# Performance work log

Hardware: AMD Instinct MI355X
Metric: run time of the kernel (lower is better)

Reference implementation:

```python
import jax, jax.numpy as jnp
import numpy as np
from jax.scipy.special import logsumexp

EPS = 1e-3
MAX_ITER = 100
THRESH = 0.1

def setup_inputs() -> dict:
    key = jax.random.key(0)
    k1, k2 = jax.random.split(key)
    B, N, M, D = 16, 1024, 1024, 32
    output = jax.random.normal(k1, (B, N, D), dtype=jnp.float32)
    labels = jax.random.normal(k2, (B, M, D), dtype=jnp.float32)
    return {"output": output, "labels": labels}

def _sinkhorn_cost(output, labels):
    # C_ij = sum_d |x_i - y_j|^2, shape [B, N, M]
    C = jnp.sum(jnp.abs(output[..., :, None, :] - labels[..., None, :, :]) ** 2, axis=-1)
    B, N, M = C.shape
    log_mu = jnp.full((B, N), jnp.log(1.0 / N + 1e-8), dtype=C.dtype)
    log_nu = jnp.full((B, M), jnp.log(1.0 / M + 1e-8), dtype=C.dtype)

    def Mmat(u, v):
        # (-C + u_i + v_j) / eps
        return (-C + u[..., :, None] + v[..., None, :]) / EPS

    def step(carry, _):
        u, v, done = carry
        u_new = EPS * (log_mu - logsumexp(Mmat(u, v), axis=-1)) + u
        v_new = EPS * (log_nu - logsumexp(Mmat(u_new, v), axis=-2)) + v
        err = jnp.mean(jnp.sum(jnp.abs(u_new - u), axis=-1))
        # the update that triggers convergence IS applied (torch breaks after update)
        u2 = jnp.where(done, u, u_new)
        v2 = jnp.where(done, v, v_new)
        done = done | (err < THRESH)
        return (u2, v2, done), None

    u0 = jnp.zeros((B, N), dtype=C.dtype)
    v0 = jnp.zeros((B, M), dtype=C.dtype)
    (u, v, _), _ = jax.lax.scan(jax.checkpoint(step), (u0, v0, jnp.asarray(False)), None, length=MAX_ITER)
    pi = jnp.exp(Mmat(u, v))
    cost = jnp.sum(pi * C, axis=(-2, -1))  # [B]
    return jnp.mean(cost)  # reduction='mean'

def reference(output, labels):
    return _sinkhorn_cost(output, labels)
```

## Files before the change

kernel.cpp:

```cpp
#include <hip/hip_runtime.h>

constexpr int   NN       = 1024;
constexpr float EPSf     = 1e-3f;
constexpr int   MAX_ITER = 100;

#define K2      1442.6950408889634f
#define TWOK2   2885.3900817779268f
#define LN2f    0.6931471805599453f
#define INV_LN2 1.4426950408889634f
#define INV_EPS 1000.0f
#define LOGK    (-6.9314616f)

#define EXP2F(x) __builtin_amdgcn_exp2f(x)
#define LOG2F(x) __builtin_amdgcn_logf(x)

typedef _Float16 f16x8 __attribute__((ext_vector_type(8)));
typedef float    f32x4 __attribute__((ext_vector_type(4)));

__device__ __forceinline__ void msmerge(float& ma, float& sa, float mb, float sb)
{
    const float m2 = fmaxf(ma, mb);
    sa = fmaf(sa, EXP2F(ma - m2), sb * EXP2F(mb - m2));
    ma = m2;
}

__global__ __launch_bounds__(256) void prep(
    const float* __restrict__ X, const float* __restrict__ Y,
    _Float16* __restrict__ Xh, _Float16* __restrict__ Yh,
    float* __restrict__ xsq, float* __restrict__ ysq)
{
    const int gid = blockIdx.x * 256 + threadIdx.x;
    const float* src; _Float16* dst; float* sq; int row;
    if (gid < 16384) { src = X; dst = Xh; sq = xsq; row = gid; }
    else             { src = Y; dst = Yh; sq = ysq; row = gid - 16384; }

    const float4* s4 = (const float4*)(src + (size_t)row * 32);
    float acc = 0.f;
#pragma unroll
    for (int i = 0; i < 4; ++i) {
        float4 a = s4[2 * i], b = s4[2 * i + 1];
        acc += a.x*a.x + a.y*a.y + a.z*a.z + a.w*a.w;
        acc += b.x*b.x + b.y*b.y + b.z*b.z + b.w*b.w;
        f16x8 h = {(_Float16)a.x, (_Float16)a.y, (_Float16)a.z, (_Float16)a.w,
                   (_Float16)b.x, (_Float16)b.y, (_Float16)b.z, (_Float16)b.w};
        *(f16x8*)(dst + (size_t)row * 32 + i * 8) = h;
    }
    sq[row] = acc;
}

#define YSLOT(c, k) (((c) << 5) + (((k) ^ (((c) >> 1) & 3)) << 3))

__global__ __launch_bounds__(1024, 1) void lse_mfma_pass(
    const _Float16* __restrict__ Ah,
    const _Float16* __restrict__ Bh,
    const float* __restrict__ asq,
    const float* __restrict__ bsq,
    const float* __restrict__ vin,
    float* __restrict__ vout,
    float* __restrict__ err,
    int* __restrict__ dflag, int it, int do_err)
{
    __shared__ _Float16 Yl[32768];
    __shared__ float    wk[1024];
    __shared__ float    mrg[64][8];
    __shared__ int      s_fb;

    const int tid = threadIdx.x;
    const int b   = blockIdx.x & 15, blk = blockIdx.x >> 4;

    if (!do_err && blockIdx.x == 0 && tid < 16) {
        float e = err[(tid << 7) + it];
        e += __shfl_xor(e, 1); e += __shfl_xor(e, 2);
        e += __shfl_xor(e, 4); e += __shfl_xor(e, 8);
        if (tid == 0) dflag[it + 1] = dflag[it] | (e < 1.6f ? 1 : 0);
    }
    if (dflag[it]) return;
    if (tid == 0) s_fb = 0;

    {
        const float4* src = (const float4*)(Bh + ((size_t)b << 15));
#pragma unroll
        for (int i = 0; i < 4; ++i) {
            const int g = tid + (i << 10);
            const int row = g >> 2, k = g & 3;
            *(float4*)(Yl + YSLOT(row, k)) = src[g];
        }
        const int c = (b << 10) + tid;
        wk[tid] = (vin[c] - bsq[c]) * K2;
    }
    __syncthreads();

    const int wave = tid >> 6, lane = tid & 63;
    const int wr = wave >> 2, wc = wave & 3;
    const int l15 = lane & 15, l4 = lane >> 4;
    const int rowb = (blk << 6) + (wr << 4);

    const f16x8 afrag = *(const f16x8*)(Ah + ((size_t)b << 15) +
                                        ((size_t)(rowb + l15) << 5) + (l4 << 3));
    const float4 xs4 = *(const float4*)(asq + (b << 10) + rowb + (l4 << 2));
    const float4 uo4 = *(const float4*)(vout + (b << 10) + rowb + (l4 << 2));
    const float xk[4] = {xs4.x * K2, xs4.y * K2, xs4.z * K2, xs4.w * K2};
    float xm[4];
    {
        const float u4[4] = {uo4.x, uo4.y, uo4.z, uo4.w};
#pragma unroll
        for (int r = 0; r < 4; ++r)
            xm[r] = xk[r] + (LOGK - u4[r] * INV_EPS) * INV_LN2;
    }

    float wreg[16];
#pragma unroll
    for (int t = 0; t < 16; ++t) wreg[t] = wk[(wc << 8) + (t << 4) + l15];

    float s[4] = {0.f, 0.f, 0.f, 0.f};
#pragma unroll 4
    for (int t = 0; t < 16; ++t) {
        const int col = (wc << 8) + (t << 4) + l15;
        const f16x8 bfrag = *(const f16x8*)(Yl + YSLOT(col, l4));
        f32x4 z = {0.f, 0.f, 0.f, 0.f};
        f32x4 d = __builtin_amdgcn_mfma_f32_16x16x32_f16(afrag, bfrag, z, 0, 0, 0);
#pragma unroll
        for (int r = 0; r < 4; ++r)
            s[r] += EXP2F(fmaf(d[r], TWOK2, wreg[t] - xm[r]));
    }
#pragma unroll
    for (int off = 1; off < 16; off <<= 1)
#pragma unroll
        for (int r = 0; r < 4; ++r) s[r] += __shfl_xor(s[r], off);
    if (l15 == 0) {
#pragma unroll
        for (int r = 0; r < 4; ++r) mrg[(wr << 4) + (l4 << 2) + r][wc] = s[r];
    }
    __syncthreads();

    float S = 0.f, uo = 0.f, M0r = 0.f;
    int gr = 0;
    if (tid < 64) {
        S = mrg[tid][0] + mrg[tid][1] + mrg[tid][2] + mrg[tid][3];
        gr = (b << 10) + (blk << 6) + tid;
        uo = vout[gr];
        M0r = (LOGK - uo * INV_EPS) * INV_LN2;
        if (!(S >= 1e-27f && S <= 1e38f)) s_fb = 1;
    }
    __syncthreads();

    if (!s_fb) {
        if (tid < 64) {
            const float lse2 = M0r + LOG2F(S);
            const float nv = EPSf * (LOGK - lse2 * LN2f);
            float werr = do_err ? fabsf(nv - uo) : 0.f;
            vout[gr] = nv;
#pragma unroll
            for (int off = 32; off > 0; off >>= 1) werr += __shfl_xor(werr, off);
            if (do_err && tid == 0) atomicAdd(err + (b << 7) + it, werr);
        }
        return;
    }

    float m[4] = {-3.4e38f, -3.4e38f, -3.4e38f, -3.4e38f};
    float sf[4] = {0.f, 0.f, 0.f, 0.f};
#pragma unroll 4
    for (int t = 0; t < 16; ++t) {
        const int col = (wc << 8) + (t << 4) + l15;
        const f16x8 bfrag = *(const f16x8*)(Yl + YSLOT(col, l4));
        f32x4 z = {0.f, 0.f, 0.f, 0.f};
        f32x4 d = __builtin_amdgcn_mfma_f32_16x16x32_f16(afrag, bfrag, z, 0, 0, 0);
#pragma unroll
        for (int r = 0; r < 4; ++r) {
            const float arg = fmaf(d[r], TWOK2, wreg[t] - xk[r]);
            const float big = fmaxf(m[r], arg);
            const float e   = EXP2F(fminf(m[r], arg) - big);
            sf[r] = (arg > m[r]) ? fmaf(sf[r], e, 1.0f) : (sf[r] + e);
            m[r] = big;
        }
    }
#pragma unroll
    for (int off = 1; off < 16; off <<= 1)
#pragma unroll
        for (int r = 0; r < 4; ++r)
            msmerge(m[r], sf[r], __shfl_xor(m[r], off), __shfl_xor(sf[r], off));
    if (l15 == 0) {
#pragma unroll
        for (int r = 0; r < 4; ++r) {
            const int rb = (wr << 4) + (l4 << 2) + r;
            mrg[rb][wc]     = m[r];
            mrg[rb][4 + wc] = sf[r];
        }
    }
    __syncthreads();

    if (tid < 64) {
        float M = mrg[tid][0], Sf = mrg[tid][4];
        msmerge(M, Sf, mrg[tid][1], mrg[tid][5]);
        msmerge(M, Sf, mrg[tid][2], mrg[tid][6]);
        msmerge(M, Sf, mrg[tid][3], mrg[tid][7]);
        const float lse2 = M + LOG2F(Sf);
        const float nv = EPSf * (LOGK - lse2 * LN2f);
        float werr = do_err ? fabsf(nv - uo) : 0.f;
        vout[gr] = nv;
#pragma unroll
        for (int off = 32; off > 0; off >>= 1) werr += __shfl_xor(werr, off);
        if (do_err && tid == 0) atomicAdd(err + (b << 7) + it, werr);
    }
}

__global__ __launch_bounds__(1024, 1) void cost_mfma(
    const _Float16* __restrict__ Xh, const _Float16* __restrict__ Yh,
    const float* __restrict__ xsq, const float* __restrict__ ysq,
    const float* __restrict__ u, const float* __restrict__ v,
    float* __restrict__ out)
{
    __shared__ _Float16 Yl[32768];
    __shared__ float red[16];
    const int tid = threadIdx.x;
    const int b   = blockIdx.x & 15, blk = blockIdx.x >> 4;

    {   const float4* src = (const float4*)(Yh + ((size_t)b << 15));
#pragma unroll
        for (int i = 0; i < 4; ++i) {
            const int g = tid + (i << 10);
            const int row = g >> 2, k = g & 3;
            *(float4*)(Yl + YSLOT(row, k)) = src[g];
        }
    }
    __syncthreads();

    const int wave = tid >> 6, lane = tid & 63;
    const int wr = wave >> 2, wc = wave & 3;
    const int l15 = lane & 15, l4 = lane >> 4;
    const int rowb = (blk << 6) + (wr << 4);

    const f16x8 afrag = *(const f16x8*)(Xh + ((size_t)b << 15) +
                                        ((size_t)(rowb + l15) << 5) + (l4 << 3));
    const float4 xs4 = *(const float4*)(xsq + (b << 10) + rowb + (l4 << 2));
    const float xs[4] = {xs4.x, xs4.y, xs4.z, xs4.w};
    const float4 uu4 = *(const float4*)(u + (b << 10) + rowb + (l4 << 2));
    const float uk[4] = {uu4.x * K2, uu4.y * K2, uu4.z * K2, uu4.w * K2};

    float vk[16], ys[16];
#pragma unroll
    for (int t = 0; t < 16; ++t) {
        const int c = (b << 10) + (wc << 8) + (t << 4) + l15;
        vk[t] = v[c] * K2;
        ys[t] = ysq[c];
    }

    float csum = 0.f;
#pragma unroll 4
    for (int t = 0; t < 16; ++t) {
        const int col = (wc << 8) + (t << 4) + l15;
        const f16x8 bfrag = *(const f16x8*)(Yl + YSLOT(col, l4));
        f32x4 z = {0.f, 0.f, 0.f, 0.f};
        f32x4 d = __builtin_amdgcn_mfma_f32_16x16x32_f16(afrag, bfrag, z, 0, 0, 0);
#pragma unroll
        for (int r = 0; r < 4; ++r) {
            const float C   = fmaf(-2.f, d[r], xs[r] + ys[t]);
            const float arg = fmaf(C, -K2, uk[r] + vk[t]);
            csum += EXP2F(arg) * C;
        }
    }
#pragma unroll
    for (int off = 32; off > 0; off >>= 1) csum += __shfl_xor(csum, off);

    if (lane == 0) red[wave] = csum;
    __syncthreads();
    if (tid == 0) {
        float tot = 0.f;
#pragma unroll
        for (int w = 0; w < 16; ++w) tot += red[w];
        atomicAdd(out, tot * (1.0f / 16.0f));
    }
}

extern "C" void kernel_launch(void* const* d_in, const int* in_sizes, int n_in,
                              void* d_out, int out_size, void* d_ws, size_t ws_size,
                              hipStream_t stream) {
    const float* x = (const float*)d_in[0];
    const float* y = (const float*)d_in[1];

    char* wsb = (char*)d_ws;
    _Float16* Xh = (_Float16*)wsb;
    _Float16* Yh = (_Float16*)(wsb + (1u << 20));
    float* xsq   = (float*)(wsb + (2u << 20));
    float* ysq   = xsq + 16384;
    float* u     = ysq + 16384;
    float* v     = u + 16384;
    float* err   = v + 16384;
    int*   dflag = (int*)(err + 2048);
    float* out   = (float*)d_out;

    (void)hipMemsetAsync(u, 0, (size_t)(2 * 16384 + 2048 + 128) * 4, stream);
    (void)hipMemsetAsync(out, 0, sizeof(float), stream);

    prep<<<dim3(128), dim3(256), 0, stream>>>(x, y, Xh, Yh, xsq, ysq);

    for (int it = 0; it < MAX_ITER; ++it) {
        lse_mfma_pass<<<dim3(256), dim3(1024), 0, stream>>>(
            Xh, Yh, xsq, ysq, v, u, err, dflag, it, 1);
        lse_mfma_pass<<<dim3(256), dim3(1024), 0, stream>>>(
            Yh, Xh, ysq, xsq, u, v, err, dflag, it, 0);
    }

    cost_mfma<<<dim3(256), dim3(1024), 0, stream>>>(Xh, Yh, xsq, ysq, u, v, out);
}
```

Before: 1.362 ms.

## Fuse u and v Sinkhorn half-steps into one kernel via column partial logsumexp

```diff
diff --git a/kernel.cpp b/kernel.cpp
--- a/kernel.cpp
+++ b/kernel.cpp
@@ -50,43 +50,61 @@
 
 #define YSLOT(c, k) (((c) << 5) + (((k) ^ (((c) >> 1) & 3)) << 3))
 
-__global__ __launch_bounds__(1024, 1) void lse_mfma_pass(
-    const _Float16* __restrict__ Ah,
-    const _Float16* __restrict__ Bh,
-    const float* __restrict__ asq,
-    const float* __restrict__ bsq,
-    const float* __restrict__ vin,
-    float* __restrict__ vout,
+__global__ __launch_bounds__(1024, 1) void sink_iter(
+    const _Float16* __restrict__ Xh, const _Float16* __restrict__ Yh,
+    const float* __restrict__ xsq, const float* __restrict__ ysq,
+    float* __restrict__ u,
+    float2* __restrict__ Sp,
     float* __restrict__ err,
-    int* __restrict__ dflag, int it, int do_err)
+    int it)
 {
     __shared__ _Float16 Yl[32768];
-    __shared__ float    wk[1024];
-    __shared__ float    mrg[64][8];
-    __shared__ int      s_fb;
+    __shared__ float  wk[1024];
+    __shared__ float  bks[1024];
+    __shared__ float  mrg[64][8];
+    __shared__ float2 colp[4][1024];
+    __shared__ float  unew[64];
+    __shared__ int    s_fb, s_frz;
 
     const int tid = threadIdx.x;
     const int b   = blockIdx.x & 15, blk = blockIdx.x >> 4;
 
-    if (!do_err && blockIdx.x == 0 && tid < 16) {
-        float e = err[(tid << 7) + it];
-        e += __shfl_xor(e, 1); e += __shfl_xor(e, 2);
-        e += __shfl_xor(e, 4); e += __shfl_xor(e, 8);
-        if (tid == 0) dflag[it + 1] = dflag[it] | (e < 1.6f ? 1 : 0);
-    }
-    if (dflag[it]) return;
+    if (it > 0) {
+        if (tid == 0) {
+            float e = 0.f;
+            const float* ep = err + (it - 1) * 16;
+#pragma unroll
+            for (int q = 0; q < 16; ++q) e += ep[q];
+            s_frz = (e < 1.6f) ? 1 : 0;
+        }
+        __syncthreads();
+        if (s_frz) return;
+    }
     if (tid == 0) s_fb = 0;
 
     {
-        const float4* src = (const float4*)(Bh + ((size_t)b << 15));
+        const float4* src = (const float4*)(Yh + ((size_t)b << 15));
 #pragma unroll
         for (int i = 0; i < 4; ++i) {
             const int g = tid + (i << 10);
             const int row = g >> 2, k = g & 3;
             *(float4*)(Yl + YSLOT(row, k)) = src[g];
         }
-        const int c = (b << 10) + tid;
-        wk[tid] = (vin[c] - bsq[c]) * K2;
+        float vj = 0.f;
+        if (it > 0) {
+            const float2* sp = Sp + ((size_t)b << 14) + tid;
+            float2 p0 = sp[0];
+            float M = p0.x, S = p0.y;
+#pragma unroll
+            for (int k = 1; k < 16; ++k) {
+                float2 p = sp[k << 10];
+                msmerge(M, S, p.x, p.y);
+            }
+            vj = EPSf * (LOGK - (M + LOG2F(S)) * LN2f);
+        }
+        const float bq = ysq[(b << 10) + tid];
+        wk[tid]  = (vj - bq) * K2;
+        bks[tid] = bq * K2;
     }
     __syncthreads();
 
@@ -95,19 +113,17 @@
     const int l15 = lane & 15, l4 = lane >> 4;
     const int rowb = (blk << 6) + (wr << 4);
 
-    const f16x8 afrag = *(const f16x8*)(Ah + ((size_t)b << 15) +
+    const f16x8 afrag = *(const f16x8*)(Xh + ((size_t)b << 15) +
                                         ((size_t)(rowb + l15) << 5) + (l4 << 3));
-    const float4 xs4 = *(const float4*)(asq + (b << 10) + rowb + (l4 << 2));
-    const float4 uo4 = *(const float4*)(vout + (b << 10) + rowb + (l4 << 2));
+    const float4 xs4 = *(const float4*)(xsq + (b << 10) + rowb + (l4 << 2));
+    const float4 uo4 = *(const float4*)(u + (b << 10) + rowb + (l4 << 2));
     const float xk[4] = {xs4.x * K2, xs4.y * K2, xs4.z * K2, xs4.w * K2};
     float xm[4];
-    {
-        const float u4[4] = {uo4.x, uo4.y, uo4.z, uo4.w};
+    {   const float u4[4] = {uo4.x, uo4.y, uo4.z, uo4.w};
 #pragma unroll
         for (int r = 0; r < 4; ++r)
             xm[r] = xk[r] + (LOGK - u4[r] * INV_EPS) * INV_LN2;
     }
-
     float wreg[16];
 #pragma unroll
     for (int t = 0; t < 16; ++t) wreg[t] = wk[(wc << 8) + (t << 4) + l15];
@@ -138,7 +154,7 @@
     if (tid < 64) {
         S = mrg[tid][0] + mrg[tid][1] + mrg[tid][2] + mrg[tid][3];
         gr = (b << 10) + (blk << 6) + tid;
-        uo = vout[gr];
+        uo = u[gr];
         M0r = (LOGK - uo * INV_EPS) * INV_LN2;
         if (!(S >= 1e-27f && S <= 1e38f)) s_fb = 1;
     }
@@ -146,19 +162,74 @@
 
     if (!s_fb) {
         if (tid < 64) {
-            const float lse2 = M0r + LOG2F(S);
-            const float nv = EPSf * (LOGK - lse2 * LN2f);
-            float werr = do_err ? fabsf(nv - uo) : 0.f;
-            vout[gr] = nv;
+            const float nv = EPSf * (LOGK - (M0r + LOG2F(S)) * LN2f);
+            unew[tid] = nv;
+            u[gr] = nv;
+            float werr = fabsf(nv - uo);
 #pragma unroll
             for (int off = 32; off > 0; off >>= 1) werr += __shfl_xor(werr, off);
-            if (do_err && tid == 0) atomicAdd(err + (b << 7) + it, werr);
-        }
-        return;
-    }
-
-    float m[4] = {-3.4e38f, -3.4e38f, -3.4e38f, -3.4e38f};
-    float sf[4] = {0.f, 0.f, 0.f, 0.f};
+            if (tid == 0) atomicAdd(err + it * 16 + b, werr);
+        }
+    } else {
+        float m[4] = {-3.4e38f, -3.4e38f, -3.4e38f, -3.4e38f};
+        float sf[4] = {0.f, 0.f, 0.f, 0.f};
+#pragma unroll 4
+        for (int t = 0; t < 16; ++t) {
+            const int col = (wc << 8) + (t << 4) + l15;
+            const f16x8 bfrag = *(const f16x8*)(Yl + YSLOT(col, l4));
+            f32x4 z = {0.f, 0.f, 0.f, 0.f};
+            f32x4 d = __builtin_amdgcn_mfma_f32_16x16x32_f16(afrag, bfrag, z, 0, 0, 0);
+#pragma unroll
+            for (int r = 0; r < 4; ++r) {
+                const float arg = fmaf(d[r], TWOK2, wreg[t] - xk[r]);
+                const float big = fmaxf(m[r], arg);
+                const float e   = EXP2F(fminf(m[r], arg) - big);
+                sf[r] = (arg > m[r]) ? fmaf(sf[r], e, 1.0f) : (sf[r] + e);
+                m[r] = big;
+            }
+        }
+#pragma unroll
+        for (int off = 1; off < 16; off <<= 1)
+#pragma unroll
+            for (int r = 0; r < 4; ++r)
+                msmerge(m[r], sf[r], __shfl_xor(m[r], off), __shfl_xor(sf[r], off));
+        if (l15 == 0) {
+#pragma unroll
+            for (int r = 0; r < 4; ++r) {
+                const int rb = (wr << 4) + (l4 << 2) + r;
+                mrg[rb][wc]     = m[r];
+                mrg[rb][4 + wc] = sf[r];
+            }
+        }
+        __syncthreads();
+        if (tid < 64) {
+            float M = mrg[tid][0], Sf = mrg[tid][4];
+            msmerge(M, Sf, mrg[tid][1], mrg[tid][5]);
+            msmerge(M, Sf, mrg[tid][2], mrg[tid][6]);
+            msmerge(M, Sf, mrg[tid][3], mrg[tid][7]);
+            const float nv = EPSf * (LOGK - (M + LOG2F(Sf)) * LN2f);
+            unew[tid] = nv;
+            u[gr] = nv;
+            float werr = fabsf(nv - uo);
+#pragma unroll
+            for (int off = 32; off > 0; off >>= 1) werr += __shfl_xor(werr, off);
+            if (tid == 0) atomicAdd(err + it * 16 + b, werr);
+        }
+    }
+    __syncthreads();
+
+    float am[4];
+#pragma unroll
+    for (int r = 0; r < 4; ++r)
+        am[r] = unew[(wr << 4) + (l4 << 2) + r] * K2 - xk[r];
+    float bkreg[16];
+#pragma unroll
+    for (int t = 0; t < 16; ++t) bkreg[t] = bks[(wc << 8) + (t << 4) + l15];
+
+    float cm[16], cs[16];
+#pragma unroll
+    for (int t = 0; t < 16; ++t) { cm[t] = -3.4e38f; cs[t] = 0.f; }
+
 #pragma unroll 4
     for (int t = 0; t < 16; ++t) {
         const int col = (wc << 8) + (t << 4) + l15;
@@ -167,50 +238,46 @@
         f32x4 d = __builtin_amdgcn_mfma_f32_16x16x32_f16(afrag, bfrag, z, 0, 0, 0);
 #pragma unroll
         for (int r = 0; r < 4; ++r) {
-            const float arg = fmaf(d[r], TWOK2, wreg[t] - xk[r]);
-            const float big = fmaxf(m[r], arg);
-            const float e   = EXP2F(fminf(m[r], arg) - big);
-            sf[r] = (arg > m[r]) ? fmaf(sf[r], e, 1.0f) : (sf[r] + e);
-            m[r] = big;
-        }
-    }
-#pragma unroll
-    for (int off = 1; off < 16; off <<= 1)
-#pragma unroll
-        for (int r = 0; r < 4; ++r)
-            msmerge(m[r], sf[r], __shfl_xor(m[r], off), __shfl_xor(sf[r], off));
-    if (l15 == 0) {
-#pragma unroll
-        for (int r = 0; r < 4; ++r) {
-            const int rb = (wr << 4) + (l4 << 2) + r;
-            mrg[rb][wc]     = m[r];
-            mrg[rb][4 + wc] = sf[r];
-        }
-    }
-    __syncthreads();
-
-    if (tid < 64) {
-        float M = mrg[tid][0], Sf = mrg[tid][4];
-        msmerge(M, Sf, mrg[tid][1], mrg[tid][5]);
-        msmerge(M, Sf, mrg[tid][2], mrg[tid][6]);
-        msmerge(M, Sf, mrg[tid][3], mrg[tid][7]);
-        const float lse2 = M + LOG2F(Sf);
-        const float nv = EPSf * (LOGK - lse2 * LN2f);
-        float werr = do_err ? fabsf(nv - uo) : 0.f;
-        vout[gr] = nv;
-#pragma unroll
-        for (int off = 32; off > 0; off >>= 1) werr += __shfl_xor(werr, off);
-        if (do_err && tid == 0) atomicAdd(err + (b << 7) + it, werr);
+            const float arg = fmaf(d[r], TWOK2, am[r] - bkreg[t]);
+            const float big = fmaxf(cm[t], arg);
+            const float e   = EXP2F(fminf(cm[t], arg) - big);
+            cs[t] = (arg > cm[t]) ? fmaf(cs[t], e, 1.0f) : (cs[t] + e);
+            cm[t] = big;
+        }
+    }
+#pragma unroll
+    for (int off = 16; off <= 32; off <<= 1)
+#pragma unroll
+        for (int t = 0; t < 16; ++t) {
+            const float mo = __shfl_xor(cm[t], off);
+            const float so = __shfl_xor(cs[t], off);
+            msmerge(cm[t], cs[t], mo, so);
+        }
+    if (l4 == 0) {
+#pragma unroll
+        for (int t = 0; t < 16; ++t)
+            colp[wr][(wc << 8) + (t << 4) + l15] = make_float2(cm[t], cs[t]);
+    }
+    __syncthreads();
+
+    {
+        float2 q0 = colp[0][tid];
+        float M = q0.x, Sv = q0.y;
+        float2 q1 = colp[1][tid]; msmerge(M, Sv, q1.x, q1.y);
+        float2 q2 = colp[2][tid]; msmerge(M, Sv, q2.x, q2.y);
+        float2 q3 = colp[3][tid]; msmerge(M, Sv, q3.x, q3.y);
+        Sp[(((size_t)b << 4) + blk << 10) + tid] = make_float2(M, Sv);
     }
 }
 
 __global__ __launch_bounds__(1024, 1) void cost_mfma(
     const _Float16* __restrict__ Xh, const _Float16* __restrict__ Yh,
     const float* __restrict__ xsq, const float* __restrict__ ysq,
-    const float* __restrict__ u, const float* __restrict__ v,
+    const float* __restrict__ u, const float2* __restrict__ Sp,
     float* __restrict__ out)
 {
     __shared__ _Float16 Yl[32768];
+    __shared__ float vkl[1024];
     __shared__ float red[16];
     const int tid = threadIdx.x;
     const int b   = blockIdx.x & 15, blk = blockIdx.x >> 4;
@@ -222,6 +289,15 @@
             const int row = g >> 2, k = g & 3;
             *(float4*)(Yl + YSLOT(row, k)) = src[g];
         }
+        const float2* sp = Sp + ((size_t)b << 14) + tid;
+        float2 p0 = sp[0];
+        float M = p0.x, S = p0.y;
+#pragma unroll
+        for (int k = 1; k < 16; ++k) {
+            float2 p = sp[k << 10];
+            msmerge(M, S, p.x, p.y);
+        }
+        vkl[tid] = EPSf * (LOGK - (M + LOG2F(S)) * LN2f) * K2;
     }
     __syncthreads();
 
@@ -240,9 +316,9 @@
     float vk[16], ys[16];
 #pragma unroll
     for (int t = 0; t < 16; ++t) {
-        const int c = (b << 10) + (wc << 8) + (t << 4) + l15;
-        vk[t] = v[c] * K2;
-        ys[t] = ysq[c];
+        const int cl = (wc << 8) + (t << 4) + l15;
+        vk[t] = vkl[cl];
+        ys[t] = ysq[(b << 10) + cl];
     }
 
     float csum = 0.f;
@@ -281,25 +357,21 @@
     char* wsb = (char*)d_ws;
     _Float16* Xh = (_Float16*)wsb;
     _Float16* Yh = (_Float16*)(wsb + (1u << 20));
-    float* xsq   = (float*)(wsb + (2u << 20));
+    float2* Sp   = (float2*)(wsb + (2u << 20));
+    float* xsq   = (float*)(wsb + (4u << 20));
     float* ysq   = xsq + 16384;
     float* u     = ysq + 16384;
-    float* v     = u + 16384;
-    float* err   = v + 16384;
-    int*   dflag = (int*)(err + 2048);
+    float* err   = u + 16384;
     float* out   = (float*)d_out;
 
-    (void)hipMemsetAsync(u, 0, (size_t)(2 * 16384 + 2048 + 128) * 4, stream);
+    (void)hipMemsetAsync(u, 0, (size_t)(16384 + 1600) * 4, stream);
     (void)hipMemsetAsync(out, 0, sizeof(float), stream);
 
     prep<<<dim3(128), dim3(256), 0, stream>>>(x, y, Xh, Yh, xsq, ysq);
 
-    for (int it = 0; it < MAX_ITER; ++it) {
-        lse_mfma_pass<<<dim3(256), dim3(1024), 0, stream>>>(
-            Xh, Yh, xsq, ysq, v, u, err, dflag, it, 1);
-        lse_mfma_pass<<<dim3(256), dim3(1024), 0, stream>>>(
-            Yh, Xh, ysq, xsq, u, v, err, dflag, it, 0);
-    }
-
-    cost_mfma<<<dim3(256), dim3(1024), 0, stream>>>(Xh, Yh, xsq, ysq, u, v, out);
-}
+    for (int it = 0; it < MAX_ITER; ++it)
+        sink_iter<<<dim3(256), dim3(1024), 0, stream>>>(
+            Xh, Yh, xsq, ysq, u, Sp, err, it);
+
+    cost_mfma<<<dim3(256), dim3(1024), 0, stream>>>(Xh, Yh, xsq, ysq, u, Sp, out);
+}
```

Result: slower. 1.947 ms (+42.9%).
